# Kernel optimization log

Measured on AMD Instinct MI355X. Metric: run time of the kernel, lower is better.

Reference implementation:

```python
import jax, jax.numpy as jnp
import numpy as np

DIM = 1024
N_HEADS = 16
D_HEAD = DIM // N_HEADS


def setup_inputs() -> dict:
    key = jax.random.key(0)
    ks = jax.random.split(key, 7)
    s = DIM ** -0.5
    return {
        "x": jax.random.normal(ks[0], (4, 2048, DIM), dtype=jnp.float32),
        "Wq": jax.random.normal(ks[1], (DIM, DIM), dtype=jnp.float32) * s,
        "bq": jax.random.normal(ks[2], (DIM,), dtype=jnp.float32) * 0.02,
        "Wk": jax.random.normal(ks[3], (DIM, DIM), dtype=jnp.float32) * s,
        "bk": jax.random.normal(ks[4], (DIM,), dtype=jnp.float32) * 0.02,
        "Wv": jax.random.normal(ks[5], (DIM, DIM), dtype=jnp.float32) * s,
        "bv": jax.random.normal(ks[6], (DIM,), dtype=jnp.float32) * 0.02,
    }


def reference(x, Wq, bq, Wk, bk, Wv, bv):
    B, N, D = x.shape
    H, Dh = N_HEADS, D_HEAD

    def split_heads(t):
        # b n (h d) -> b h n d
        return t.reshape(B, N, H, Dh).transpose(0, 2, 1, 3)

    q = split_heads(x @ Wq + bq)
    k = split_heads(x @ Wk + bk)
    v = split_heads(x @ Wv + bv)

    scale = Dh ** -0.5
    logit = jnp.einsum("bhnd,bhmd->bhnm", q, k) * scale  # [B,H,N,N]
    attn = jax.nn.softmax(logit, axis=-1)
    out = jnp.einsum("bhnm,bhmd->bhnd", attn, v)
    # b h n d -> b n (h d)
    return out.transpose(0, 2, 1, 3).reshape(B, N, D)
```

## Files before the change

kernel.cpp:

```cpp
#include <hip/hip_runtime.h>
#include <hip/hip_bf16.h>
#include <stdint.h>

#define BB 4
#define SEQ 2048
#define DIM 1024
#define NH 16
#define DH 64
#define MM (BB*SEQ)

typedef unsigned short u16;
typedef __attribute__((ext_vector_type(8))) __bf16 bf16x8;
typedef __attribute__((ext_vector_type(4))) float floatx4;
typedef __attribute__((ext_vector_type(4))) unsigned short u16x4;
typedef __attribute__((ext_vector_type(4))) short short4v;

#define QSCALE 0.18033688011112042f

__device__ __forceinline__ u16 f2bf(float f) {
    union { float f; unsigned u; } v; v.f = f;
    unsigned u = v.u;
    u += 0x7FFF + ((u >> 16) & 1);
    return (u16)(u >> 16);
}

__device__ __forceinline__ bf16x8 ldb8(const u16* p) {
    return *(const bf16x8*)(const void*)p;
}

__device__ __forceinline__ void async_copy16(const u16* g, u16* l) {
    __builtin_amdgcn_global_load_lds(
        (const __attribute__((address_space(1))) unsigned int*)g,
        (__attribute__((address_space(3))) unsigned int*)l, 16, 0, 0);
}

__device__ __forceinline__ floatx4 mfma16(short4v a, short4v b, floatx4 c) {
    return __builtin_amdgcn_mfma_f32_16x16x16bf16_1k(a, b, c, 0, 0, 0);
}

__global__ __launch_bounds__(256)
void prep(const float* __restrict__ x, u16* __restrict__ xb,
          const float* __restrict__ Wq, const float* __restrict__ Wk,
          const float* __restrict__ Wv, u16* __restrict__ Wt) {
    const int bx = blockIdx.x;
    const int tid = threadIdx.x;
    if (bx < 8192) {
        const size_t i = ((size_t)bx * 256 + tid) * 4;
        float4 f = *(const float4*)(x + i);
        u16x4 o = { f2bf(f.x), f2bf(f.y), f2bf(f.z), f2bf(f.w) };
        *(u16x4*)(xb + i) = o;
        return;
    }
    const int idx = bx - 8192;
    const int t = idx >> 8;
    const int r2 = idx & 255;
    const int k0 = (r2 >> 4) * 64, n0 = (r2 & 15) * 64;
    const float* W = (t == 0) ? Wq : (t == 1) ? Wk : Wv;
    u16* D = Wt + (size_t)t * DIM * DIM;
    __shared__ u16 T[64][65];
    #pragma unroll
    for (int p = 0; p < 4; p++) {
        const int r = p * 16 + (tid >> 4), c = (tid & 15) * 4;
        float4 f = *(const float4*)(W + (size_t)(k0 + r) * DIM + n0 + c);
        T[c + 0][r] = f2bf(f.x); T[c + 1][r] = f2bf(f.y);
        T[c + 2][r] = f2bf(f.z); T[c + 3][r] = f2bf(f.w);
    }
    __syncthreads();
    #pragma unroll
    for (int p = 0; p < 4; p++) {
        const int rn = p * 16 + (tid >> 4), ck = (tid & 15) * 4;
        u16x4 v = { T[rn][ck], T[rn][ck + 1], T[rn][ck + 2], T[rn][ck + 3] };
        *(u16x4*)(D + (size_t)(n0 + rn) * DIM + k0 + ck) = v;
    }
}

__global__ __launch_bounds__(256, 3)
void qkv_gemm3(const u16* __restrict__ xb, const u16* __restrict__ Wt,
               const float* __restrict__ bq, const float* __restrict__ bk,
               const float* __restrict__ bv, u16* __restrict__ ws) {
    __shared__ u16 As[2][4096];
    __shared__ u16 Bs[2][4096];

    const int m0 = blockIdx.x * 128;
    const int t  = blockIdx.y >> 3;
    const int c0 = (blockIdx.y & 7) * 128;
    const u16* Wtb = Wt + (size_t)t * DIM * DIM;
    const float* bias = (t == 0) ? bq : (t == 1) ? bk : bv;
    const float osc = (t == 0) ? QSCALE : 1.0f;
    u16* dst = ws + (size_t)t * ((size_t)MM * DIM);

    const int tid  = threadIdx.x;
    const int lane = tid & 63;
    const int w    = tid >> 6;
    const int wr = w >> 1, wc = w & 1;
    const int g = lane >> 4, ln = lane & 15;

    floatx4 acc[4][4];
    #pragma unroll
    for (int i = 0; i < 4; i++)
        #pragma unroll
        for (int j = 0; j < 4; j++) acc[i][j] = (floatx4){0.f,0.f,0.f,0.f};

    const int srow = w*16 + (lane >> 2);
    const int gseg = (lane & 3) ^ ((lane >> 3) & 3);
    const u16* gA = xb  + (size_t)(m0 + srow) * DIM + gseg*8;
    const u16* gB = Wtb + (size_t)(c0 + srow) * DIM + gseg*8;

    async_copy16(gA,                   &As[0][w*512]);
    async_copy16(gA + (size_t)64*DIM,  &As[0][2048 + w*512]);
    async_copy16(gB,                   &Bs[0][w*512]);
    async_copy16(gB + (size_t)64*DIM,  &Bs[0][2048 + w*512]);
    __syncthreads();

    const int xu = (ln >> 1) & 3;

    for (int it = 0; it < 32; it++) {
        const int cur = it & 1;
        if (it < 31) {
            const int nxt = cur ^ 1;
            const int kk = (it + 1) * 32;
            async_copy16(gA + kk,                  &As[nxt][w*512]);
            async_copy16(gA + kk + (size_t)64*DIM, &As[nxt][2048 + w*512]);
            async_copy16(gB + kk,                  &Bs[nxt][w*512]);
            async_copy16(gB + kk + (size_t)64*DIM, &Bs[nxt][2048 + w*512]);
        }

        bf16x8 a[4], b[4];
        #pragma unroll
        for (int fr = 0; fr < 4; fr++)
            a[fr] = ldb8(&As[cur][(wr*64 + fr*16 + ln)*32 + (g ^ xu)*8]);
        #pragma unroll
        for (int fc = 0; fc < 4; fc++)
            b[fc] = ldb8(&Bs[cur][(wc*64 + fc*16 + ln)*32 + (g ^ xu)*8]);

        if (t < 2) {
            #pragma unroll
            for (int fr = 0; fr < 4; fr++)
                #pragma unroll
                for (int fc = 0; fc < 4; fc++)
                    acc[fr][fc] = __builtin_amdgcn_mfma_f32_16x16x32_bf16(
                        b[fc], a[fr], acc[fr][fc], 0, 0, 0);
        } else {
            #pragma unroll
            for (int fr = 0; fr < 4; fr++)
                #pragma unroll
                for (int fc = 0; fc < 4; fc++)
                    acc[fr][fc] = __builtin_amdgcn_mfma_f32_16x16x32_bf16(
                        a[fr], b[fc], acc[fr][fc], 0, 0, 0);
        }
        __syncthreads();
    }

    if (t < 2) {
        #pragma unroll
        for (int fc = 0; fc < 4; fc++) {
            const int cc = c0 + wc*64 + fc*16 + g*4;
            const float4 b4 = *(const float4*)&bias[cc];
            const int h = cc >> 6, d = cc & 63;
            #pragma unroll
            for (int fr = 0; fr < 4; fr++) {
                const int tok = m0 + wr*64 + fr*16 + ln;
                const int bidx = tok >> 11, nn = tok & 2047;
                u16x4 v = { f2bf((acc[fr][fc][0] + b4.x) * osc),
                            f2bf((acc[fr][fc][1] + b4.y) * osc),
                            f2bf((acc[fr][fc][2] + b4.z) * osc),
                            f2bf((acc[fr][fc][3] + b4.w) * osc) };
                *(u16x4*)&dst[((size_t)(bidx*NH + h)*SEQ + nn)*DH + d] = v;
            }
        }
    } else {
        #pragma unroll
        for (int fc = 0; fc < 4; fc++) {
            const int cc = c0 + wc*64 + fc*16 + ln;
            const float bias_v = bias[cc];
            const int h = cc >> 6, d = cc & 63;
            #pragma unroll
            for (int fr = 0; fr < 4; fr++) {
                const int mrow = m0 + wr*64 + fr*16 + g*4;
                const int bidx = mrow >> 11, nn = mrow & 2047;
                u16x4 v = { f2bf(acc[fr][fc][0] + bias_v), f2bf(acc[fr][fc][1] + bias_v),
                            f2bf(acc[fr][fc][2] + bias_v), f2bf(acc[fr][fc][3] + bias_v) };
                *(u16x4*)&dst[((size_t)(bidx*NH + h)*DH + d)*SEQ + nn] = v;
            }
        }
    }
}

#define LDA 40
__global__ __launch_bounds__(256)
void qkv_gemm(const float* __restrict__ x,
              const float* __restrict__ Wq, const float* __restrict__ bq,
              const float* __restrict__ Wk, const float* __restrict__ bk,
              const float* __restrict__ Wv, const float* __restrict__ bv,
              u16* __restrict__ ws) {
    __shared__ u16 As[128 * LDA];
    __shared__ u16 Bs[128 * LDA];
    const int m0 = blockIdx.x * 128;
    const int t  = blockIdx.y >> 3;
    const int c0 = (blockIdx.y & 7) * 128;
    const float* W    = (t == 0) ? Wq : (t == 1) ? Wk : Wv;
    const float* bias = (t == 0) ? bq : (t == 1) ? bk : bv;
    const float osc = (t == 0) ? QSCALE : 1.0f;
    u16* dst = ws + (size_t)t * ((size_t)MM * DIM);
    const int tid  = threadIdx.x;
    const int lane = tid & 63;
    const int wave = tid >> 6;
    const int wr = wave >> 1, wc = wave & 1;
    const int g = lane >> 4, ln = lane & 15;
    floatx4 acc[4][4];
    #pragma unroll
    for (int i = 0; i < 4; i++)
        #pragma unroll
        for (int j = 0; j < 4; j++) acc[i][j] = (floatx4){0.f,0.f,0.f,0.f};
    const int ar  = tid >> 1;
    const int ak  = (tid & 1) * 16;
    const int bkr = tid & 31;
    const int bc  = (tid >> 5) * 16;
    for (int kk = 0; kk < DIM; kk += 32) {
        {
            const float4* s4 = (const float4*)(x + (size_t)(m0 + ar) * DIM + kk + ak);
            float4 f0 = s4[0], f1 = s4[1], f2 = s4[2], f3 = s4[3];
            unsigned pk[8];
            pk[0] = f2bf(f0.x) | ((unsigned)f2bf(f0.y) << 16);
            pk[1] = f2bf(f0.z) | ((unsigned)f2bf(f0.w) << 16);
            pk[2] = f2bf(f1.x) | ((unsigned)f2bf(f1.y) << 16);
            pk[3] = f2bf(f1.z) | ((unsigned)f2bf(f1.w) << 16);
            pk[4] = f2bf(f2.x) | ((unsigned)f2bf(f2.y) << 16);
            pk[5] = f2bf(f2.z) | ((unsigned)f2bf(f2.w) << 16);
            pk[6] = f2bf(f3.x) | ((unsigned)f2bf(f3.y) << 16);
            pk[7] = f2bf(f3.z) | ((unsigned)f2bf(f3.w) << 16);
            uint4* d = (uint4*)&As[ar * LDA + ak];
            d[0] = make_uint4(pk[0], pk[1], pk[2], pk[3]);
            d[1] = make_uint4(pk[4], pk[5], pk[6], pk[7]);
        }
        {
            const float4* s4 = (const float4*)(W + (size_t)(kk + bkr) * DIM + c0 + bc);
            float4 f0 = s4[0], f1 = s4[1], f2 = s4[2], f3 = s4[3];
            float fv[16] = {f0.x,f0.y,f0.z,f0.w, f1.x,f1.y,f1.z,f1.w,
                            f2.x,f2.y,f2.z,f2.w, f3.x,f3.y,f3.z,f3.w};
            #pragma unroll
            for (int j = 0; j < 16; j++)
                Bs[(bc + j) * LDA + bkr] = f2bf(fv[j]);
        }
        __syncthreads();
        bf16x8 a[4], b[4];
        #pragma unroll
        for (int fr = 0; fr < 4; fr++)
            a[fr] = ldb8(&As[(wr*64 + fr*16 + ln) * LDA + g*8]);
        #pragma unroll
        for (int fc = 0; fc < 4; fc++)
            b[fc] = ldb8(&Bs[(wc*64 + fc*16 + ln) * LDA + g*8]);
        #pragma unroll
        for (int fr = 0; fr < 4; fr++)
            #pragma unroll
            for (int fc = 0; fc < 4; fc++)
                acc[fr][fc] = __builtin_amdgcn_mfma_f32_16x16x32_bf16(
                    a[fr], b[fc], acc[fr][fc], 0, 0, 0);
        __syncthreads();
    }
    #pragma unroll
    for (int fc = 0; fc < 4; fc++) {
        const int cc = c0 + wc*64 + fc*16 + ln;
        const float bias_v = bias[cc];
        const int h = cc >> 6, d = cc & 63;
        #pragma unroll
        for (int fr = 0; fr < 4; fr++) {
            #pragma unroll
            for (int rr = 0; rr < 4; rr++) {
                const int mrow = m0 + wr*64 + fr*16 + g*4 + rr;
                const int bidx = mrow >> 11, nn = mrow & 2047;
                const float val = (acc[fr][fc][rr] + bias_v) * osc;
                size_t idx;
                if (t < 2) idx = ((size_t)(bidx*NH + h)*SEQ + nn)*DH + d;
                else       idx = ((size_t)(bidx*NH + h)*DH + d)*SEQ + nn;
                dst[idx] = f2bf(val);
            }
        }
    }
}

__global__ __launch_bounds__(512, 8)
void attn7(const u16* __restrict__ ws, float* __restrict__ out) {
    const int qt = blockIdx.x;
    const int h  = blockIdx.y;
    const int b  = blockIdx.z;
    const int bh = b*NH + h;

    const u16* Qw = ws;
    const u16* Kw = ws + (size_t)MM * DIM;
    const u16* Vt = ws + 2 * (size_t)MM * DIM;

    __shared__ u16 Kbuf[2][4096];
    __shared__ u16 Vbuf[2][4096];

    const int tid  = threadIdx.x;
    const int lane = tid & 63;
    const int w    = tid >> 6;
    const int g = lane >> 4, ln = lane & 15;
    const int q0 = qt*128 + w*16;

    const int srow = w*8 + (lane >> 3);
    const int sseg = (lane & 7) ^ ((lane >> 3) & 7);
    const u16* kg = Kw + ((size_t)bh*SEQ + srow)*DH + sseg*8;
    const u16* vg = Vt + ((size_t)bh*DH + srow)*SEQ + sseg*8;

    const int fs0 = ((0*4 + g) ^ (ln & 7)) * 8;
    const int fs1 = ((1*4 + g) ^ (ln & 7)) * 8;
    const int vxor = ln & 7;
    const int gh = g >> 1;
    const int vh = (g & 1) * 4;

    bf16x8 aq0, aq1;
    {
        const u16* qp = Qw + ((size_t)bh*SEQ + q0 + ln)*DH + g*8;
        aq0 = ldb8(qp);
        aq1 = ldb8(qp + 32);
    }

    floatx4 acc[4];
    #pragma unroll
    for (int i = 0; i < 4; i++) acc[i] = (floatx4){0.f,0.f,0.f,0.f};
    float lrun = 0.f;

    async_copy16(kg, &Kbuf[0][w*512]);
    async_copy16(vg, &Vbuf[0][w*512]);
    __syncthreads();

    for (int kt = 0; kt < 32; kt++) {
        const int cur = kt & 1;
        if (kt < 31) {
            const int nxt = cur ^ 1;
            const size_t ko = (size_t)(kt + 1) * 64 * DH;
            const size_t vo = (size_t)(kt + 1) * 64;
            async_copy16(kg + ko, &Kbuf[nxt][w*512]);
            async_copy16(vg + vo, &Vbuf[nxt][w*512]);
        }

        const u16* Kc = &Kbuf[cur][0];
        const u16* Vc = &Vbuf[cur][0];

        #pragma unroll
        for (int fn = 0; fn < 4; fn++) {
            bf16x8 k0 = ldb8(&Kc[(fn*16 + ln)*64 + fs0]);
            bf16x8 k1 = ldb8(&Kc[(fn*16 + ln)*64 + fs1]);
            floatx4 z = (floatx4){0.f,0.f,0.f,0.f};
            z = __builtin_amdgcn_mfma_f32_16x16x32_bf16(k0, aq0, z, 0, 0, 0);
            z = __builtin_amdgcn_mfma_f32_16x16x32_bf16(k1, aq1, z, 0, 0, 0);
            float p0 = __builtin_amdgcn_exp2f(z[0]);
            float p1 = __builtin_amdgcn_exp2f(z[1]);
            float p2 = __builtin_amdgcn_exp2f(z[2]);
            float p3 = __builtin_amdgcn_exp2f(z[3]);
            lrun += (p0 + p1) + (p2 + p3);
            union { __hip_bfloat162 h2[2]; short4v s4; } pu;
            pu.h2[0] = __float22bfloat162_rn(make_float2(p0, p1));
            pu.h2[1] = __float22bfloat162_rn(make_float2(p2, p3));
            const short4v bp = pu.s4;

            const int vu = ((fn*2 + gh) ^ vxor) * 8 + vh;
            #pragma unroll
            for (int fd = 0; fd < 4; fd++) {
                short4v av = *(const short4v*)(const void*)&Vc[(fd*16 + ln)*64 + vu];
                acc[fd] = mfma16(av, bp, acc[fd]);
            }
        }
        __syncthreads();
    }

    {
        float v = lrun;
        v += __shfl_xor(v, 16, 64);
        v += __shfl_xor(v, 32, 64);
        const float inv = 1.0f / v;
        const int n = q0 + ln;
        #pragma unroll
        for (int fd = 0; fd < 4; fd++) {
            floatx4 vv = acc[fd];
            float4 o = { vv[0]*inv, vv[1]*inv, vv[2]*inv, vv[3]*inv };
            *(float4*)&out[((size_t)b*SEQ + n)*DIM + h*DH + fd*16 + g*4] = o;
        }
    }
}

extern "C" void kernel_launch(void* const* d_in, const int* in_sizes, int n_in,
                              void* d_out, int out_size, void* d_ws, size_t ws_size,
                              hipStream_t stream) {
    const float* x  = (const float*)d_in[0];
    const float* Wq = (const float*)d_in[1];
    const float* bq = (const float*)d_in[2];
    const float* Wk = (const float*)d_in[3];
    const float* bk = (const float*)d_in[4];
    const float* Wv = (const float*)d_in[5];
    const float* bv = (const float*)d_in[6];
    u16* ws = (u16*)d_ws;
    float* out = (float*)d_out;

    const size_t need = (size_t)4 * MM * DIM * 2 + (size_t)3 * DIM * DIM * 2;
    if (ws_size >= need) {
        u16* xb = ws + (size_t)3 * MM * DIM;
        u16* Wt = ws + (size_t)4 * MM * DIM;
        prep<<<dim3(8192 + 768), 256, 0, stream>>>(x, xb, Wq, Wk, Wv, Wt);
        qkv_gemm3<<<dim3(MM/128, 24), 256, 0, stream>>>(xb, Wt, bq, bk, bv, ws);
    } else {
        qkv_gemm<<<dim3(MM/128, 24), 256, 0, stream>>>(x, Wq, bq, Wk, bk, Wv, bv, ws);
    }
    attn7<<<dim3(SEQ/128, NH, BB), 512, 0, stream>>>(ws, out);
}
```

Measured before the change: 277.2 us.

## Switch attention to 32x32 MFMA tiles with 256-query blocks

Rewrites the attention kernel to use 32x32x16 bf16 MFMA for both QK^T and PV, with each wave owning 32 query rows and each block covering 256 queries. The probability tile is converted to bf16 and rearranged across half-waves with permlane32_swap so it can serve directly as the PV operand, which avoids an LDS round trip. Each K/V tile loaded into LDS is now reused by twice as many queries, and larger MFMAs mean fewer instructions. In exchange, per-thread accumulator registers grow, launch bounds drop to 4 blocks per CU, and the grid halves to 512 blocks, which lowers occupancy.

```diff
diff --git a/kernel.cpp b/kernel.cpp
--- a/kernel.cpp
+++ b/kernel.cpp
@@ -12,8 +12,9 @@
 typedef unsigned short u16;
 typedef __attribute__((ext_vector_type(8))) __bf16 bf16x8;
 typedef __attribute__((ext_vector_type(4))) float floatx4;
+typedef __attribute__((ext_vector_type(16))) float floatx16;
 typedef __attribute__((ext_vector_type(4))) unsigned short u16x4;
-typedef __attribute__((ext_vector_type(4))) short short4v;
+typedef __attribute__((ext_vector_type(2))) unsigned int uint2v;
 
 #define QSCALE 0.18033688011112042f
 
@@ -34,8 +35,8 @@
         (__attribute__((address_space(3))) unsigned int*)l, 16, 0, 0);
 }
 
-__device__ __forceinline__ floatx4 mfma16(short4v a, short4v b, floatx4 c) {
-    return __builtin_amdgcn_mfma_f32_16x16x16bf16_1k(a, b, c, 0, 0, 0);
+__device__ __forceinline__ floatx16 mfma32(bf16x8 a, bf16x8 b, floatx16 c) {
+    return __builtin_amdgcn_mfma_f32_32x32x16_bf16(a, b, c, 0, 0, 0);
 }
 
 __global__ __launch_bounds__(256)
@@ -279,8 +280,8 @@
     }
 }
 
-__global__ __launch_bounds__(512, 8)
-void attn7(const u16* __restrict__ ws, float* __restrict__ out) {
+__global__ __launch_bounds__(512, 4)
+void attn8(const u16* __restrict__ ws, float* __restrict__ out) {
     const int qt = blockIdx.x;
     const int h  = blockIdx.y;
     const int b  = blockIdx.z;
@@ -296,30 +297,28 @@
     const int tid  = threadIdx.x;
     const int lane = tid & 63;
     const int w    = tid >> 6;
-    const int g = lane >> 4, ln = lane & 15;
-    const int q0 = qt*128 + w*16;
+    const int l31  = lane & 31;
+    const int hi   = lane >> 5;
+    const int c7   = lane & 7;
+    const int q0w  = qt*256 + w*32;
 
     const int srow = w*8 + (lane >> 3);
     const int sseg = (lane & 7) ^ ((lane >> 3) & 7);
     const u16* kg = Kw + ((size_t)bh*SEQ + srow)*DH + sseg*8;
     const u16* vg = Vt + ((size_t)bh*DH + srow)*SEQ + sseg*8;
 
-    const int fs0 = ((0*4 + g) ^ (ln & 7)) * 8;
-    const int fs1 = ((1*4 + g) ^ (ln & 7)) * 8;
-    const int vxor = ln & 7;
-    const int gh = g >> 1;
-    const int vh = (g & 1) * 4;
-
-    bf16x8 aq0, aq1;
+    bf16x8 qf[4];
     {
-        const u16* qp = Qw + ((size_t)bh*SEQ + q0 + ln)*DH + g*8;
-        aq0 = ldb8(qp);
-        aq1 = ldb8(qp + 32);
-    }
-
-    floatx4 acc[4];
-    #pragma unroll
-    for (int i = 0; i < 4; i++) acc[i] = (floatx4){0.f,0.f,0.f,0.f};
+        const u16* qp = Qw + ((size_t)bh*SEQ + q0w + l31)*DH + hi*8;
+        #pragma unroll
+        for (int ds = 0; ds < 4; ds++) qf[ds] = ldb8(qp + ds*16);
+    }
+
+    floatx16 accO[2];
+    #pragma unroll
+    for (int fd = 0; fd < 2; fd++)
+        #pragma unroll
+        for (int r = 0; r < 16; r++) accO[fd][r] = 0.f;
     float lrun = 0.f;
 
     async_copy16(kg, &Kbuf[0][w*512]);
@@ -330,37 +329,51 @@
         const int cur = kt & 1;
         if (kt < 31) {
             const int nxt = cur ^ 1;
-            const size_t ko = (size_t)(kt + 1) * 64 * DH;
-            const size_t vo = (size_t)(kt + 1) * 64;
-            async_copy16(kg + ko, &Kbuf[nxt][w*512]);
-            async_copy16(vg + vo, &Vbuf[nxt][w*512]);
+            async_copy16(kg + (size_t)(kt + 1) * 64 * DH, &Kbuf[nxt][w*512]);
+            async_copy16(vg + (size_t)(kt + 1) * 64,      &Vbuf[nxt][w*512]);
         }
 
         const u16* Kc = &Kbuf[cur][0];
         const u16* Vc = &Vbuf[cur][0];
 
         #pragma unroll
-        for (int fn = 0; fn < 4; fn++) {
-            bf16x8 k0 = ldb8(&Kc[(fn*16 + ln)*64 + fs0]);
-            bf16x8 k1 = ldb8(&Kc[(fn*16 + ln)*64 + fs1]);
-            floatx4 z = (floatx4){0.f,0.f,0.f,0.f};
-            z = __builtin_amdgcn_mfma_f32_16x16x32_bf16(k0, aq0, z, 0, 0, 0);
-            z = __builtin_amdgcn_mfma_f32_16x16x32_bf16(k1, aq1, z, 0, 0, 0);
-            float p0 = __builtin_amdgcn_exp2f(z[0]);
-            float p1 = __builtin_amdgcn_exp2f(z[1]);
-            float p2 = __builtin_amdgcn_exp2f(z[2]);
-            float p3 = __builtin_amdgcn_exp2f(z[3]);
-            lrun += (p0 + p1) + (p2 + p3);
-            union { __hip_bfloat162 h2[2]; short4v s4; } pu;
-            pu.h2[0] = __float22bfloat162_rn(make_float2(p0, p1));
-            pu.h2[1] = __float22bfloat162_rn(make_float2(p2, p3));
-            const short4v bp = pu.s4;
-
-            const int vu = ((fn*2 + gh) ^ vxor) * 8 + vh;
-            #pragma unroll
-            for (int fd = 0; fd < 4; fd++) {
-                short4v av = *(const short4v*)(const void*)&Vc[(fd*16 + ln)*64 + vu];
-                acc[fd] = mfma16(av, bp, acc[fd]);
+        for (int kb = 0; kb < 2; kb++) {
+            floatx16 z;
+            #pragma unroll
+            for (int r = 0; r < 16; r++) z[r] = 0.f;
+            #pragma unroll
+            for (int ds = 0; ds < 4; ds++) {
+                bf16x8 kf = ldb8(&Kc[(kb*32 + l31)*64 + ((ds*2 + hi) ^ c7)*8]);
+                z = mfma32(kf, qf[ds], z);
+            }
+
+            float p[16];
+            #pragma unroll
+            for (int r = 0; r < 16; r++) {
+                p[r] = __builtin_amdgcn_exp2f(z[r]);
+                lrun += p[r];
+            }
+            unsigned c[8];
+            #pragma unroll
+            for (int i = 0; i < 8; i++) {
+                union { __hip_bfloat162 h2; unsigned u; } pu;
+                pu.h2 = __float22bfloat162_rn(make_float2(p[2*i], p[2*i+1]));
+                c[i] = pu.u;
+            }
+            uint2v s02 = __builtin_amdgcn_permlane32_swap(c[0], c[2], false, false);
+            uint2v s13 = __builtin_amdgcn_permlane32_swap(c[1], c[3], false, false);
+            uint2v s46 = __builtin_amdgcn_permlane32_swap(c[4], c[6], false, false);
+            uint2v s57 = __builtin_amdgcn_permlane32_swap(c[5], c[7], false, false);
+            union { unsigned u[4]; bf16x8 v; } bp0, bp1;
+            bp0.u[0] = s02[0]; bp0.u[1] = s13[0]; bp0.u[2] = s02[1]; bp0.u[3] = s13[1];
+            bp1.u[0] = s46[0]; bp1.u[1] = s57[0]; bp1.u[2] = s46[1]; bp1.u[3] = s57[1];
+
+            #pragma unroll
+            for (int fd = 0; fd < 2; fd++) {
+                bf16x8 av0 = ldb8(&Vc[(fd*32 + l31)*64 + ((kb*4 + 0 + hi) ^ c7)*8]);
+                accO[fd] = mfma32(av0, bp0.v, accO[fd]);
+                bf16x8 av1 = ldb8(&Vc[(fd*32 + l31)*64 + ((kb*4 + 2 + hi) ^ c7)*8]);
+                accO[fd] = mfma32(av1, bp1.v, accO[fd]);
             }
         }
         __syncthreads();
@@ -368,16 +381,19 @@
 
     {
         float v = lrun;
-        v += __shfl_xor(v, 16, 64);
         v += __shfl_xor(v, 32, 64);
         const float inv = 1.0f / v;
-        const int n = q0 + ln;
-        #pragma unroll
-        for (int fd = 0; fd < 4; fd++) {
-            floatx4 vv = acc[fd];
-            float4 o = { vv[0]*inv, vv[1]*inv, vv[2]*inv, vv[3]*inv };
-            *(float4*)&out[((size_t)b*SEQ + n)*DIM + h*DH + fd*16 + g*4] = o;
-        }
+        const int n = q0w + l31;
+        float* orow = &out[((size_t)b*SEQ + n)*DIM + h*DH];
+        #pragma unroll
+        for (int fd = 0; fd < 2; fd++)
+            #pragma unroll
+            for (int rp = 0; rp < 4; rp++) {
+                const int d = fd*32 + rp*8 + hi*4;
+                float4 o = { accO[fd][rp*4+0]*inv, accO[fd][rp*4+1]*inv,
+                             accO[fd][rp*4+2]*inv, accO[fd][rp*4+3]*inv };
+                *(float4*)&orow[d] = o;
+            }
     }
 }
 
@@ -403,5 +419,5 @@
     } else {
         qkv_gemm<<<dim3(MM/128, 24), 256, 0, stream>>>(x, Wq, bq, Wk, bk, Wv, bv, ws);
     }
-    attn7<<<dim3(SEQ/128, NH, BB), 512, 0, stream>>>(ws, out);
-}
+    attn8<<<dim3(SEQ/256, NH, BB), 512, 0, stream>>>(ws, out);
+}
```

Result: faster. 259.0 us (-6.6%).
